# Performance work log

Measured on AMD Instinct MI355X. Metric: run time of the kernel, lower is better.

Reference implementation:

```python
import jax, jax.numpy as jnp
import numpy as np

D_MODEL = 2048
N_HEADS = 32
N_KV = 8
D_K = D_MODEL // N_HEADS  # 64
N_REP = N_HEADS // N_KV   # 4


def setup_inputs() -> dict:
    key = jax.random.key(0)
    ks = jax.random.split(key, 5)
    B, T = 2, 2048
    s = 0.02
    return {
        "x": jax.random.normal(ks[0], (B, T, D_MODEL), dtype=jnp.float32),
        "Wq": jax.random.normal(ks[1], (D_MODEL, D_MODEL), dtype=jnp.float32) * s,
        "Wk": jax.random.normal(ks[2], (N_KV * D_K, D_MODEL), dtype=jnp.float32) * s,
        "Wv": jax.random.normal(ks[3], (N_KV * D_K, D_MODEL), dtype=jnp.float32) * s,
        "Wo": jax.random.normal(ks[4], (D_MODEL, D_MODEL), dtype=jnp.float32) * s,
    }


def reference(x, Wq, Wk, Wv, Wo):
    B, T, C = x.shape
    # projections (torch Linear: x @ W.T)
    Q = (x @ Wq.T).reshape(B, T, N_KV, N_REP, D_K)  # group query heads by kv group
    K = (x @ Wk.T).reshape(B, T, N_KV, D_K)
    V = (x @ Wv.T).reshape(B, T, N_KV, D_K)
    scale = 1.0 / jnp.sqrt(jnp.asarray(D_K, dtype=x.dtype))
    # scores: (B, n_kv, n_rep, T, T) == repeated-KV scores without materializing repeats
    scores = jnp.einsum('btgrd,bsgd->bgrts', Q, K) * scale
    causal_mask = jnp.triu(jnp.ones((T, T), dtype=bool), k=1)
    scores = jnp.where(causal_mask, -jnp.inf, scores)
    attn = jax.nn.softmax(scores, axis=-1)
    out = jnp.einsum('bgrts,bsgd->btgrd', attn, V).reshape(B, T, C)
    return out @ Wo.T
```

## Files before the change

### kernel.cpp

```cpp
#include <hip/hip_runtime.h>
#include <hip/hip_bf16.h>

typedef __attribute__((ext_vector_type(8))) short bf16x8;
typedef __attribute__((ext_vector_type(4))) float floatx4;

constexpr int D_MODEL = 2048;
constexpr int N_HEADS = 32;
constexpr int N_KV    = 8;
constexpr int B_      = 2;
constexpr int T_      = 2048;
constexpr int BT      = B_ * T_;
constexpr int NQKV    = 3072;

constexpr float Q_SCALE = 0.18033688011112042f;

__device__ __forceinline__ unsigned short f2bf(float f) {
    __hip_bfloat16 h = __float2bfloat16(f);
    return *reinterpret_cast<unsigned short*>(&h);
}

__device__ __forceinline__ void gll16(const void* g, void* l) {
    typedef const __attribute__((address_space(1))) unsigned int* gp_t;
    typedef __attribute__((address_space(3))) unsigned int* lp_t;
    __builtin_amdgcn_global_load_lds((gp_t)g, (lp_t)l, 16, 0, 0);
}

__global__ __launch_bounds__(256) void cvt_all(
        const float* __restrict__ x,  const float* __restrict__ wq,
        const float* __restrict__ wk, const float* __restrict__ wv,
        unsigned short* __restrict__ dst) {
    size_t i4 = (size_t)blockIdx.x * 256 + threadIdx.x;
    size_t e = i4 * 4;
    const float* src; size_t off;
    if (e < 8388608)        { src = x;  off = 0; }
    else if (e < 12582912)  { src = wq; off = 8388608; }
    else if (e < 13631488)  { src = wk; off = 12582912; }
    else                    { src = wv; off = 13631488; }
    float4 f = *reinterpret_cast<const float4*>(src + (e - off));
    unsigned short u[4] = {f2bf(f.x), f2bf(f.y), f2bf(f.z), f2bf(f.w)};
    reinterpret_cast<uint2*>(dst)[i4] = *reinterpret_cast<const uint2*>(u);
}

__global__ __launch_bounds__(256) void cvt_bf16(
        const float* __restrict__ src, unsigned short* __restrict__ dst, int n4) {
    int i = blockIdx.x * 256 + threadIdx.x;
    if (i < n4) {
        float4 f = reinterpret_cast<const float4*>(src)[i];
        unsigned short u[4] = {f2bf(f.x), f2bf(f.y), f2bf(f.z), f2bf(f.w)};
        reinterpret_cast<uint2*>(dst)[i] = *reinterpret_cast<const uint2*>(u);
    }
}

template<bool C_F32, bool SCALEQ>
__global__ __launch_bounds__(256) void gemm128(
        const unsigned short* __restrict__ A,
        const unsigned short* __restrict__ Bb,
        void* __restrict__ Cp,
        int M, int N, int K) {
    __shared__ unsigned short As[128 * 64];
    __shared__ unsigned short Bs[128 * 64];
    const int t = threadIdx.x;
    const int wave = t >> 6, lane = t & 63;
    const int l16 = lane & 15, quad = lane >> 4;
    const int wm = (wave & 1) * 64, wn = (wave >> 1) * 64;
    const int mtile = blockIdx.y * 128, ntile = blockIdx.x * 128;

    floatx4 acc[4][4] = {};

    for (int k0 = 0; k0 < K; k0 += 64) {
        __syncthreads();
#pragma unroll
        for (int c = 0; c < 4; c++) {
            int s = (c * 4 + wave) * 64 + lane;
            int row = s >> 3, k8 = (s & 7) ^ (row & 7);
            gll16(&A[(size_t)(mtile + row) * K + k0 + k8 * 8], &As[(c * 4 + wave) * 512]);
            gll16(&Bb[(size_t)(ntile + row) * K + k0 + k8 * 8], &Bs[(c * 4 + wave) * 512]);
        }
        __syncthreads();
#pragma unroll
        for (int kc = 0; kc < 2; kc++) {
            bf16x8 af[4], bfr[4];
#pragma unroll
            for (int i = 0; i < 4; i++) {
                int arow = wm + i * 16 + l16;
                af[i] = *reinterpret_cast<const bf16x8*>(
                    &As[(arow * 8 + ((kc * 4 + quad) ^ (arow & 7))) * 8]);
                int brow = wn + i * 16 + l16;
                bfr[i] = *reinterpret_cast<const bf16x8*>(
                    &Bs[(brow * 8 + ((kc * 4 + quad) ^ (brow & 7))) * 8]);
            }
#pragma unroll
            for (int i = 0; i < 4; i++)
#pragma unroll
                for (int jn = 0; jn < 4; jn++)
                    acc[i][jn] = __builtin_amdgcn_mfma_f32_16x16x32_bf16(
                        af[i], bfr[jn], acc[i][jn], 0, 0, 0);
        }
    }
    float cscale = (SCALEQ && ntile < 2048) ? Q_SCALE : 1.0f;
#pragma unroll
    for (int i = 0; i < 4; i++)
#pragma unroll
        for (int jn = 0; jn < 4; jn++)
#pragma unroll
            for (int r = 0; r < 4; r++) {
                int row = mtile + wm + i * 16 + quad * 4 + r;
                int col = ntile + wn + jn * 16 + l16;
                if constexpr (C_F32)
                    ((float*)Cp)[(size_t)row * N + col] = acc[i][jn][r];
                else
                    ((unsigned short*)Cp)[(size_t)row * N + col] =
                        f2bf(acc[i][jn][r] * cscale);
            }
}

__global__ __launch_bounds__(256) void vtrans(
        const unsigned short* __restrict__ QKV,
        unsigned short* __restrict__ Vt) {
    __shared__ unsigned short Ts[64][72];
    const int tb = blockIdx.x * 64;
    const int bg = blockIdx.y;
    const int b = bg >> 3, g = bg & 7;
    const int t = threadIdx.x;
#pragma unroll
    for (int it = 0; it < 2; it++) {
        int row = (t >> 3) + it * 32;
        int sl = t & 7;
        *reinterpret_cast<uint4*>(&Ts[row][sl * 8]) =
            *reinterpret_cast<const uint4*>(
                &QKV[(size_t)(b * T_ + tb + row) * NQKV + 2560 + g * 64 + sl * 8]);
    }
    __syncthreads();
#pragma unroll
    for (int it = 0; it < 2; it++) {
        int d = (t >> 3) + it * 32;
        int ks = t & 7;
        unsigned short u[8];
#pragma unroll
        for (int j = 0; j < 8; j++) u[j] = Ts[ks * 8 + j][d];
        *reinterpret_cast<uint4*>(&Vt[((size_t)bg * 64 + d) * T_ + tb + ks * 8]) =
            *reinterpret_cast<const uint4*>(u);
    }
}

__global__ __launch_bounds__(256, 2) void attn5(
        const unsigned short* __restrict__ QKV,
        const unsigned short* __restrict__ Vt,
        unsigned short* __restrict__ O) {
    __shared__ unsigned short Ks[64 * 64];
    __shared__ unsigned short Vs[64 * 64];
    __shared__ unsigned short Ps[4][32 * 72];
    const int j  = blockIdx.x;
    const int bh = blockIdx.y;
    const int b = bh >> 5, h = bh & 31;
    const int g = h >> 2;
    const int t = threadIdx.x, wave = t >> 6, lane = t & 63;
    const int l16 = lane & 15, quad = lane >> 4;

    bf16x8 ones;
#pragma unroll
    for (int i = 0; i < 8; i++) ones[i] = (short)0x3F80;

    for (int pp = 0; pp < 2; pp++) {
        const int qtl = pp ? (15 - j) : j;
        const int q0  = qtl * 128;
        const int qlo = q0 + wave * 32;

        bf16x8 qf[2][2];
#pragma unroll
        for (int qb = 0; qb < 2; qb++) {
            const unsigned short* qptr =
                QKV + (size_t)(b * T_ + qlo + qb * 16 + l16) * NQKV + h * 64;
            qf[qb][0] = *reinterpret_cast<const bf16x8*>(qptr + quad * 8);
            qf[qb][1] = *reinterpret_cast<const bf16x8*>(qptr + 32 + quad * 8);
        }

        floatx4 o[2][4] = {};
        floatx4 lacc[2] = {};

        const int nkt = 2 * qtl + 2;
        for (int kt = 0; kt < nkt; kt++) {
            const int kb = kt * 64;
            __syncthreads();
#pragma unroll
            for (int c = 0; c < 2; c++) {
                int s = (c * 4 + wave) * 64 + lane;
                int row = s >> 3, k8 = (s & 7) ^ (row & 7);
                gll16(&QKV[(size_t)(b * T_ + kb + row) * NQKV + 2048 + g * 64 + k8 * 8],
                      &Ks[(c * 4 + wave) * 512]);
                gll16(&Vt[((size_t)(b * 8 + g) * 64 + row) * T_ + kb + k8 * 8],
                      &Vs[(c * 4 + wave) * 512]);
            }
            __syncthreads();

            if (kb > qlo + 31) continue;
            const bool needmask = (kb + 63 > qlo);

#pragma unroll
            for (int km = 0; km < 4; km++) {
                int krow = km * 16 + l16;
                bf16x8 k0 = *reinterpret_cast<const bf16x8*>(
                    &Ks[(krow * 8 + (quad ^ (krow & 7))) * 8]);
                bf16x8 k1 = *reinterpret_cast<const bf16x8*>(
                    &Ks[(krow * 8 + ((4 + quad) ^ (krow & 7))) * 8]);
#pragma unroll
                for (int qb = 0; qb < 2; qb++) {
                    floatx4 z = {};
                    z = __builtin_amdgcn_mfma_f32_16x16x32_bf16(k0, qf[qb][0], z, 0, 0, 0);
                    z = __builtin_amdgcn_mfma_f32_16x16x32_bf16(k1, qf[qb][1], z, 0, 0, 0);
                    unsigned short u[4];
                    if (needmask) {
                        int qq = qlo + qb * 16 + l16;
#pragma unroll
                        for (int r = 0; r < 4; r++) {
                            float p = __builtin_amdgcn_exp2f(z[r]);
                            if ((kb + km * 16 + quad * 4 + r) > qq) p = 0.f;
                            u[r] = f2bf(p);
                        }
                    } else {
#pragma unroll
                        for (int r = 0; r < 4; r++)
                            u[r] = f2bf(__builtin_amdgcn_exp2f(z[r]));
                    }
                    *reinterpret_cast<uint2*>(
                        &Ps[wave][(qb * 16 + l16) * 72 + km * 16 + quad * 4]) =
                        *reinterpret_cast<const uint2*>(u);
                }
            }

            bf16x8 pf[2][2];
#pragma unroll
            for (int qb = 0; qb < 2; qb++) {
#pragma unroll
                for (int ks = 0; ks < 2; ks++)
                    pf[qb][ks] = *reinterpret_cast<const bf16x8*>(
                        &Ps[wave][(qb * 16 + l16) * 72 + ks * 32 + quad * 8]);
                lacc[qb] = __builtin_amdgcn_mfma_f32_16x16x32_bf16(
                    pf[qb][0], ones, lacc[qb], 0, 0, 0);
                lacc[qb] = __builtin_amdgcn_mfma_f32_16x16x32_bf16(
                    pf[qb][1], ones, lacc[qb], 0, 0, 0);
            }
#pragma unroll
            for (int dt = 0; dt < 4; dt++) {
                int vrow = dt * 16 + l16;
                bf16x8 v0 = *reinterpret_cast<const bf16x8*>(
                    &Vs[(vrow * 8 + (quad ^ (vrow & 7))) * 8]);
                bf16x8 v1 = *reinterpret_cast<const bf16x8*>(
                    &Vs[(vrow * 8 + ((4 + quad) ^ (vrow & 7))) * 8]);
#pragma unroll
                for (int qb = 0; qb < 2; qb++) {
                    o[qb][dt] = __builtin_amdgcn_mfma_f32_16x16x32_bf16(
                        pf[qb][0], v0, o[qb][dt], 0, 0, 0);
                    o[qb][dt] = __builtin_amdgcn_mfma_f32_16x16x32_bf16(
                        pf[qb][1], v1, o[qb][dt], 0, 0, 0);
                }
            }
        }

#pragma unroll
        for (int qb = 0; qb < 2; qb++)
#pragma unroll
            for (int r = 0; r < 4; r++) {
                float inv = 1.0f / lacc[qb][r];
                int row = b * T_ + qlo + qb * 16 + quad * 4 + r;
#pragma unroll
                for (int dt = 0; dt < 4; dt++)
                    O[(size_t)row * D_MODEL + h * 64 + dt * 16 + l16] =
                        f2bf(o[qb][dt][r] * inv);
            }
    }
}

extern "C" void kernel_launch(void* const* d_in, const int* in_sizes, int n_in,
                              void* d_out, int out_size, void* d_ws, size_t ws_size,
                              hipStream_t stream) {
    const float* x  = (const float*)d_in[0];
    const float* Wq = (const float*)d_in[1];
    const float* Wk = (const float*)d_in[2];
    const float* Wv = (const float*)d_in[3];
    const float* Wo = (const float*)d_in[4];

    unsigned short* xb   = (unsigned short*)d_ws;
    unsigned short* Wqkv = xb + (size_t)BT * D_MODEL;
    unsigned short* QKVo = Wqkv + (size_t)NQKV * D_MODEL;
    unsigned short* Vt   = QKVo + (size_t)BT * NQKV;
    unsigned short* Aw   = xb;
    unsigned short* Wob  = Wqkv;

    dim3 blk(256);
    cvt_all<<<dim3(14336), blk, 0, stream>>>(x, Wq, Wk, Wv, xb);
    gemm128<false, true><<<dim3(NQKV / 128, BT / 128), blk, 0, stream>>>(
        xb, Wqkv, QKVo, BT, NQKV, D_MODEL);
    cvt_bf16<<<dim3(D_MODEL * D_MODEL / 4 / 256), blk, 0, stream>>>(
        Wo, Wob, D_MODEL * D_MODEL / 4);
    vtrans<<<dim3(T_ / 64, B_ * N_KV), blk, 0, stream>>>(QKVo, Vt);
    attn5<<<dim3(8, B_ * N_HEADS), blk, 0, stream>>>(QKVo, Vt, Aw);
    gemm128<true, false><<<dim3(D_MODEL / 128, BT / 128), blk, 0, stream>>>(
        Aw, Wob, d_out, BT, D_MODEL, D_MODEL);
}
```

Baseline: 281.8 us.

## Double-buffer K/V tiles in attention and launch one query tile per block

The attention kernel now prefetches the next K and V tiles into a second LDS buffer while the current tile is being computed. That drops one barrier per iteration and hides global load latency behind MFMA work. Blocks now handle a single 128-row query tile instead of a light/heavy pair, with the heaviest tiles scheduled first. The launch-bounds occupancy hint rises from 2 to 3 blocks per CU. LDS use per block roughly grows to about 50KB, which could limit how many blocks actually fit per CU, and the tighter register budget may cause spills.

```diff
diff --git a/kernel.cpp b/kernel.cpp
--- a/kernel.cpp
+++ b/kernel.cpp
@@ -143,15 +143,15 @@
     }
 }
 
-__global__ __launch_bounds__(256, 2) void attn5(
+__global__ __launch_bounds__(256, 3) void attn6(
         const unsigned short* __restrict__ QKV,
         const unsigned short* __restrict__ Vt,
         unsigned short* __restrict__ O) {
-    __shared__ unsigned short Ks[64 * 64];
-    __shared__ unsigned short Vs[64 * 64];
+    __shared__ unsigned short Ks[2][64 * 64];
+    __shared__ unsigned short Vs[2][64 * 64];
     __shared__ unsigned short Ps[4][32 * 72];
-    const int j  = blockIdx.x;
-    const int bh = blockIdx.y;
+    const int qtl = 15 - blockIdx.x;
+    const int bh  = blockIdx.y;
     const int b = bh >> 5, h = bh & 31;
     const int g = h >> 2;
     const int t = threadIdx.x, wave = t >> 6, lane = t & 63;
@@ -161,114 +161,126 @@
 #pragma unroll
     for (int i = 0; i < 8; i++) ones[i] = (short)0x3F80;
 
-    for (int pp = 0; pp < 2; pp++) {
-        const int qtl = pp ? (15 - j) : j;
-        const int q0  = qtl * 128;
-        const int qlo = q0 + wave * 32;
-
-        bf16x8 qf[2][2];
-#pragma unroll
-        for (int qb = 0; qb < 2; qb++) {
-            const unsigned short* qptr =
-                QKV + (size_t)(b * T_ + qlo + qb * 16 + l16) * NQKV + h * 64;
-            qf[qb][0] = *reinterpret_cast<const bf16x8*>(qptr + quad * 8);
-            qf[qb][1] = *reinterpret_cast<const bf16x8*>(qptr + 32 + quad * 8);
-        }
-
-        floatx4 o[2][4] = {};
-        floatx4 lacc[2] = {};
-
-        const int nkt = 2 * qtl + 2;
-        for (int kt = 0; kt < nkt; kt++) {
-            const int kb = kt * 64;
-            __syncthreads();
+    const int q0  = qtl * 128;
+    const int qlo = q0 + wave * 32;
+
+    bf16x8 qf[2][2];
+#pragma unroll
+    for (int qb = 0; qb < 2; qb++) {
+        const unsigned short* qptr =
+            QKV + (size_t)(b * T_ + qlo + qb * 16 + l16) * NQKV + h * 64;
+        qf[qb][0] = *reinterpret_cast<const bf16x8*>(qptr + quad * 8);
+        qf[qb][1] = *reinterpret_cast<const bf16x8*>(qptr + 32 + quad * 8);
+    }
+
+    floatx4 o[2][4] = {};
+    floatx4 lacc[2] = {};
+
+    const int nkt = 2 * qtl + 2;
+
+#pragma unroll
+    for (int c = 0; c < 2; c++) {
+        int s = (c * 4 + wave) * 64 + lane;
+        int row = s >> 3, k8 = (s & 7) ^ (row & 7);
+        gll16(&QKV[(size_t)(b * T_ + row) * NQKV + 2048 + g * 64 + k8 * 8],
+              &Ks[0][(c * 4 + wave) * 512]);
+        gll16(&Vt[((size_t)(b * 8 + g) * 64 + row) * T_ + k8 * 8],
+              &Vs[0][(c * 4 + wave) * 512]);
+    }
+
+    for (int kt = 0; kt < nkt; kt++) {
+        const int kb = kt * 64;
+        const int cur = kt & 1;
+        __syncthreads();
+        if (kt + 1 < nkt) {
+            const int kb1 = kb + 64;
+            const int nxt = cur ^ 1;
 #pragma unroll
             for (int c = 0; c < 2; c++) {
                 int s = (c * 4 + wave) * 64 + lane;
                 int row = s >> 3, k8 = (s & 7) ^ (row & 7);
-                gll16(&QKV[(size_t)(b * T_ + kb + row) * NQKV + 2048 + g * 64 + k8 * 8],
-                      &Ks[(c * 4 + wave) * 512]);
-                gll16(&Vt[((size_t)(b * 8 + g) * 64 + row) * T_ + kb + k8 * 8],
-                      &Vs[(c * 4 + wave) * 512]);
-            }
-            __syncthreads();
-
-            if (kb > qlo + 31) continue;
-            const bool needmask = (kb + 63 > qlo);
-
-#pragma unroll
-            for (int km = 0; km < 4; km++) {
-                int krow = km * 16 + l16;
-                bf16x8 k0 = *reinterpret_cast<const bf16x8*>(
-                    &Ks[(krow * 8 + (quad ^ (krow & 7))) * 8]);
-                bf16x8 k1 = *reinterpret_cast<const bf16x8*>(
-                    &Ks[(krow * 8 + ((4 + quad) ^ (krow & 7))) * 8]);
-#pragma unroll
-                for (int qb = 0; qb < 2; qb++) {
-                    floatx4 z = {};
-                    z = __builtin_amdgcn_mfma_f32_16x16x32_bf16(k0, qf[qb][0], z, 0, 0, 0);
-                    z = __builtin_amdgcn_mfma_f32_16x16x32_bf16(k1, qf[qb][1], z, 0, 0, 0);
-                    unsigned short u[4];
-                    if (needmask) {
-                        int qq = qlo + qb * 16 + l16;
-#pragma unroll
-                        for (int r = 0; r < 4; r++) {
-                            float p = __builtin_amdgcn_exp2f(z[r]);
-                            if ((kb + km * 16 + quad * 4 + r) > qq) p = 0.f;
-                            u[r] = f2bf(p);
-                        }
-                    } else {
-#pragma unroll
-                        for (int r = 0; r < 4; r++)
-                            u[r] = f2bf(__builtin_amdgcn_exp2f(z[r]));
+                gll16(&QKV[(size_t)(b * T_ + kb1 + row) * NQKV + 2048 + g * 64 + k8 * 8],
+                      &Ks[nxt][(c * 4 + wave) * 512]);
+                gll16(&Vt[((size_t)(b * 8 + g) * 64 + row) * T_ + kb1 + k8 * 8],
+                      &Vs[nxt][(c * 4 + wave) * 512]);
+            }
+        }
+
+        if (kb > qlo + 31) continue;
+        const bool needmask = (kb + 63 > qlo);
+
+#pragma unroll
+        for (int km = 0; km < 4; km++) {
+            int krow = km * 16 + l16;
+            bf16x8 k0 = *reinterpret_cast<const bf16x8*>(
+                &Ks[cur][(krow * 8 + (quad ^ (krow & 7))) * 8]);
+            bf16x8 k1 = *reinterpret_cast<const bf16x8*>(
+                &Ks[cur][(krow * 8 + ((4 + quad) ^ (krow & 7))) * 8]);
+#pragma unroll
+            for (int qb = 0; qb < 2; qb++) {
+                floatx4 z = {};
+                z = __builtin_amdgcn_mfma_f32_16x16x32_bf16(k0, qf[qb][0], z, 0, 0, 0);
+                z = __builtin_amdgcn_mfma_f32_16x16x32_bf16(k1, qf[qb][1], z, 0, 0, 0);
+                unsigned short u[4];
+                if (needmask) {
+                    int qq = qlo + qb * 16 + l16;
+#pragma unroll
+                    for (int r = 0; r < 4; r++) {
+                        float p = __builtin_amdgcn_exp2f(z[r]);
+                        if ((kb + km * 16 + quad * 4 + r) > qq) p = 0.f;
+                        u[r] = f2bf(p);
                     }
-                    *reinterpret_cast<uint2*>(
-                        &Ps[wave][(qb * 16 + l16) * 72 + km * 16 + quad * 4]) =
-                        *reinterpret_cast<const uint2*>(u);
+                } else {
+#pragma unroll
+                    for (int r = 0; r < 4; r++)
+                        u[r] = f2bf(__builtin_amdgcn_exp2f(z[r]));
                 }
-            }
-
-            bf16x8 pf[2][2];
+                *reinterpret_cast<uint2*>(
+                    &Ps[wave][(qb * 16 + l16) * 72 + km * 16 + quad * 4]) =
+                    *reinterpret_cast<const uint2*>(u);
+            }
+        }
+
+        bf16x8 pf[2][2];
+#pragma unroll
+        for (int qb = 0; qb < 2; qb++) {
+#pragma unroll
+            for (int ks = 0; ks < 2; ks++)
+                pf[qb][ks] = *reinterpret_cast<const bf16x8*>(
+                    &Ps[wave][(qb * 16 + l16) * 72 + ks * 32 + quad * 8]);
+            lacc[qb] = __builtin_amdgcn_mfma_f32_16x16x32_bf16(
+                pf[qb][0], ones, lacc[qb], 0, 0, 0);
+            lacc[qb] = __builtin_amdgcn_mfma_f32_16x16x32_bf16(
+                pf[qb][1], ones, lacc[qb], 0, 0, 0);
+        }
+#pragma unroll
+        for (int dt = 0; dt < 4; dt++) {
+            int vrow = dt * 16 + l16;
+            bf16x8 v0 = *reinterpret_cast<const bf16x8*>(
+                &Vs[cur][(vrow * 8 + (quad ^ (vrow & 7))) * 8]);
+            bf16x8 v1 = *reinterpret_cast<const bf16x8*>(
+                &Vs[cur][(vrow * 8 + ((4 + quad) ^ (vrow & 7))) * 8]);
 #pragma unroll
             for (int qb = 0; qb < 2; qb++) {
-#pragma unroll
-                for (int ks = 0; ks < 2; ks++)
-                    pf[qb][ks] = *reinterpret_cast<const bf16x8*>(
-                        &Ps[wave][(qb * 16 + l16) * 72 + ks * 32 + quad * 8]);
-                lacc[qb] = __builtin_amdgcn_mfma_f32_16x16x32_bf16(
-                    pf[qb][0], ones, lacc[qb], 0, 0, 0);
-                lacc[qb] = __builtin_amdgcn_mfma_f32_16x16x32_bf16(
-                    pf[qb][1], ones, lacc[qb], 0, 0, 0);
-            }
-#pragma unroll
-            for (int dt = 0; dt < 4; dt++) {
-                int vrow = dt * 16 + l16;
-                bf16x8 v0 = *reinterpret_cast<const bf16x8*>(
-                    &Vs[(vrow * 8 + (quad ^ (vrow & 7))) * 8]);
-                bf16x8 v1 = *reinterpret_cast<const bf16x8*>(
-                    &Vs[(vrow * 8 + ((4 + quad) ^ (vrow & 7))) * 8]);
-#pragma unroll
-                for (int qb = 0; qb < 2; qb++) {
-                    o[qb][dt] = __builtin_amdgcn_mfma_f32_16x16x32_bf16(
-                        pf[qb][0], v0, o[qb][dt], 0, 0, 0);
-                    o[qb][dt] = __builtin_amdgcn_mfma_f32_16x16x32_bf16(
-                        pf[qb][1], v1, o[qb][dt], 0, 0, 0);
-                }
-            }
-        }
-
-#pragma unroll
-        for (int qb = 0; qb < 2; qb++)
-#pragma unroll
-            for (int r = 0; r < 4; r++) {
-                float inv = 1.0f / lacc[qb][r];
-                int row = b * T_ + qlo + qb * 16 + quad * 4 + r;
-#pragma unroll
-                for (int dt = 0; dt < 4; dt++)
-                    O[(size_t)row * D_MODEL + h * 64 + dt * 16 + l16] =
-                        f2bf(o[qb][dt][r] * inv);
-            }
-    }
+                o[qb][dt] = __builtin_amdgcn_mfma_f32_16x16x32_bf16(
+                    pf[qb][0], v0, o[qb][dt], 0, 0, 0);
+                o[qb][dt] = __builtin_amdgcn_mfma_f32_16x16x32_bf16(
+                    pf[qb][1], v1, o[qb][dt], 0, 0, 0);
+            }
+        }
+    }
+
+#pragma unroll
+    for (int qb = 0; qb < 2; qb++)
+#pragma unroll
+        for (int r = 0; r < 4; r++) {
+            float inv = 1.0f / lacc[qb][r];
+            int row = b * T_ + qlo + qb * 16 + quad * 4 + r;
+#pragma unroll
+            for (int dt = 0; dt < 4; dt++)
+                O[(size_t)row * D_MODEL + h * 64 + dt * 16 + l16] =
+                    f2bf(o[qb][dt][r] * inv);
+        }
 }
 
 extern "C" void kernel_launch(void* const* d_in, const int* in_sizes, int n_in,
@@ -294,7 +306,7 @@
     cvt_bf16<<<dim3(D_MODEL * D_MODEL / 4 / 256), blk, 0, stream>>>(
         Wo, Wob, D_MODEL * D_MODEL / 4);
     vtrans<<<dim3(T_ / 64, B_ * N_KV), blk, 0, stream>>>(QKVo, Vt);
-    attn5<<<dim3(8, B_ * N_HEADS), blk, 0, stream>>>(QKVo, Vt, Aw);
+    attn6<<<dim3(16, B_ * N_HEADS), blk, 0, stream>>>(QKVo, Vt, Aw);
     gemm128<true, false><<<dim3(D_MODEL / 128, BT / 128), blk, 0, stream>>>(
         Aw, Wob, d_out, BT, D_MODEL, D_MODEL);
 }
```

Measured after the change: 328.6 us. 1.17x slower.
